# Kernel tuning notes

Measured on AMD Instinct MI355X. Metric: run time of the kernel, lower is better.

## Reference

```python
import jax, jax.numpy as jnp
import numpy as np

B, P, C = 2, 2048, 64
SIZE = 128          # image_size
K = 8               # points_per_pixel (z-buffer depth)
RADIUS = 1.5        # in pixels
RAD_POW = 2
TAU = 1.0
BIG = 1e10          # sentinel z for pixels a point does not cover


def setup_inputs() -> dict:
    key = jax.random.key(0)
    k1, k2, k3 = jax.random.split(key, 3)
    xy = jax.random.uniform(k1, (B, P, 2), minval=-1.0, maxval=1.0)   # NDC xy
    z = jax.random.uniform(k2, (B, P, 1), minval=0.1, maxval=10.0)    # depth > 0
    pts3D = jnp.concatenate([xy, z], axis=-1)                          # [B,P,3]
    src = jax.random.normal(k3, (B, C, P), dtype=jnp.float32)          # [B,C,P]
    return {"pts3D": pts3D, "src": src}


def reference(pts3D, src):
    # --- sign flips from the torch forward: pts[:, :, :2] *= -1 ---
    pts = pts3D * jnp.array([-1.0, -1.0, 1.0], dtype=pts3D.dtype)
    px, py, pz = pts[..., 0], pts[..., 1], pts[..., 2]                 # [B,P]

    r_ndc = float(RADIUS) / float(SIZE) * 2.0

    # pixel-center NDC grid (pytorch3d convention: +x left, +y up)
    ii = jnp.arange(SIZE, dtype=pts.dtype)
    ndc = 1.0 - 2.0 * (ii + 0.5) / SIZE                                # [SIZE]

    # squared NDC distance pixel->point: [B,H,W,P]
    dx = ndc[None, None, :, None] - px[:, None, None, :]               # [B,1,W,P]
    dy = ndc[None, :, None, None] - py[:, None, None, :]               # [B,H,1,P]
    d2 = dx * dx + dy * dy                                             # [B,H,W,P]

    # rasterize_points: per pixel, K nearest-in-z points within radius
    inside = d2 <= r_ndc * r_ndc
    zkey = jnp.where(inside, pz[:, None, None, :], jnp.asarray(BIG, d2.dtype))
    neg_top, idx = jax.lax.top_k(-zkey, K)            # smallest z first, [B,H,W,K]
    valid = (-neg_top) < BIG                           # idx >= 0 equivalent

    dist = jnp.take_along_axis(d2, idx, axis=-1)       # [B,H,W,K]
    dist = dist / (r_ndc ** RAD_POW)

    # alphas = (1 - clamp(dist,0.001,1)^0.5)^tau
    alphas = (1.0 - jnp.sqrt(jnp.clip(dist, 0.001, 1.0))) ** TAU
    alphas = jnp.where(valid, alphas, 0.0)

    # alpha_composite: w_k = a_k * prod_{j<k} (1 - a_j), front-to-back
    T = jnp.cumprod(1.0 - alphas, axis=-1)
    w = alphas * jnp.concatenate([jnp.ones_like(T[..., :1]), T[..., :-1]], axis=-1)

    # gather features per batch: src [B,C,P], idx [B,H,W,K] -> [B,C,H,W,K]
    gathered = jax.vmap(lambda f, i: f[:, i])(src, idx)
    out = jnp.einsum('bchwk,bhwk->bchw', gathered, w)  # [B,C,H,W]
    return out
```

## Files before the change

### kernel.cpp

```cpp
#include <hip/hip_runtime.h>
#include <hip/hip_bf16.h>

#define BATCH 2
#define NPTS 2048
#define NCH 64
#define IMG 128
#define KTOP 8
#define BIGF 1e10f
#define CAP 256

__global__ __launch_bounds__(256) void transpose_src(
    const float* __restrict__ src, float* __restrict__ srcT) {
  __shared__ float tile[64][65];
  int b = blockIdx.x >> 5;
  int p0 = (blockIdx.x & 31) << 6;
  int tx = threadIdx.x & 63;
  int ty = threadIdx.x >> 6;
  const float* s = src + b * NCH * NPTS;
  #pragma unroll
  for (int cc = 0; cc < 64; cc += 4) {
    int c = cc + ty;
    tile[tx][c] = s[c * NPTS + p0 + tx];
  }
  __syncthreads();
  float* dT = srcT + (b * NPTS + p0) * NCH;
  #pragma unroll
  for (int pp = 0; pp < 64; pp += 4) {
    int p = pp + ty;
    dT[p * NCH + tx] = tile[p][tx];
  }
}

__global__ __launch_bounds__(256) void raster_fused(
    const float* __restrict__ pts,
    const float* __restrict__ srcT,
    float* __restrict__ out) {
  __shared__ float4 cand[CAP];
  __shared__ int cnt_s;

  const int bid = blockIdx.x;
  const int b = bid >> 8;
  const int h = (bid >> 1) & 127;
  const int w0 = (bid & 1) << 6;
  const int tid = threadIdx.x;

  if (tid == 0) cnt_s = 0;
  __syncthreads();

  const float r_ndc = 0.0234375f;
  const float r2 = r_ndc * r_ndc;
  const float yc = 1.0f - 2.0f * (h + 0.5f) / 128.0f;

  const float* pb = pts + b * NPTS * 3;
  for (int p = tid; p < NPTS; p += 256) {
    float y = pb[p * 3 + 1];
    float dy = yc + y;
    if (dy * dy <= r2) {
      int pos = atomicAdd(&cnt_s, 1);
      if (pos < CAP)
        cand[pos] = make_float4(pb[p * 3 + 0], y, pb[p * 3 + 2],
                                __int_as_float(p));
    }
  }
  __syncthreads();
  const int cnt = min(cnt_s, CAP);

  const int pix = tid & 63;
  const int w = w0 + pix;
  const float xc = 1.0f - 2.0f * (w + 0.5f) / 128.0f;

  float bz[KTOP], bd[KTOP];
  int bi[KTOP];
  #pragma unroll
  for (int k = 0; k < KTOP; ++k) { bz[k] = BIGF; bd[k] = 0.f; bi[k] = 0x7fffffff; }

  for (int j = 0; j < cnt; ++j) {
    float4 c4 = cand[j];
    float dx = xc + c4.x;
    float dyy = yc + c4.y;
    float d2 = dx * dx + dyy * dyy;
    if (d2 <= r2) {
      float cz = c4.z, cd = d2;
      int ci = __float_as_int(c4.w);
      #pragma unroll
      for (int s = 0; s < KTOP; ++s) {
        bool lt = (cz < bz[s]) || (cz == bz[s] && ci < bi[s]);
        float tz = bz[s], td = bd[s];
        int ti = bi[s];
        if (lt) { bz[s] = cz; bd[s] = cd; bi[s] = ci; cz = tz; cd = td; ci = ti; }
      }
    }
  }

  float wgt[KTOP];
  float T = 1.0f;
  const float inv_r2 = 1.0f / r2;
  #pragma unroll
  for (int k = 0; k < KTOP; ++k) {
    float alpha = 0.0f;
    if (bz[k] < BIGF) {
      float dist = bd[k] * inv_r2;
      dist = fminf(fmaxf(dist, 0.001f), 1.0f);
      alpha = 1.0f - sqrtf(dist);
    } else {
      bi[k] = 0;
    }
    wgt[k] = alpha * T;
    T *= (1.0f - alpha);
  }

  const float4* sb = (const float4*)(srcT + b * NPTS * NCH);
  const float4* rows[KTOP];
  #pragma unroll
  for (int k = 0; k < KTOP; ++k) rows[k] = sb + bi[k] * (NCH / 4);

  const int cq0 = (tid >> 6) * 4;
  float* ob = out + (b * NCH * IMG + h) * IMG + w;
  #pragma unroll
  for (int q = 0; q < 4; ++q) {
    int cq = cq0 + q;
    float4 acc = {0.f, 0.f, 0.f, 0.f};
    #pragma unroll
    for (int k = 0; k < KTOP; ++k) {
      float4 v = rows[k][cq];
      acc.x += wgt[k] * v.x;
      acc.y += wgt[k] * v.y;
      acc.z += wgt[k] * v.z;
      acc.w += wgt[k] * v.w;
    }
    int c = cq * 4;
    ob[(c + 0) * (IMG * IMG)] = acc.x;
    ob[(c + 1) * (IMG * IMG)] = acc.y;
    ob[(c + 2) * (IMG * IMG)] = acc.z;
    ob[(c + 3) * (IMG * IMG)] = acc.w;
  }
}

extern "C" void kernel_launch(void* const* d_in, const int* in_sizes, int n_in,
                              void* d_out, int out_size, void* d_ws, size_t ws_size,
                              hipStream_t stream) {
  const float* pts = (const float*)d_in[0];
  const float* src = (const float*)d_in[1];
  float* out = (float*)d_out;
  float* srcT = (float*)d_ws;

  transpose_src<<<BATCH * (NPTS / 64), 256, 0, stream>>>(src, srcT);
  raster_fused<<<BATCH * IMG * 2, 256, 0, stream>>>(pts, srcT, out);
}
```

Baseline: 88.58 us.

## Drop transpose kernel; stage candidate features in shared memory per row block

Removes the separate transpose kernel and its launch. Each raster block now gathers the features of its candidate points directly from the channel-major src into a padded shared-memory table. The top-K tracking carries a local candidate index, so the final weighted sum reads from LDS instead of making scattered global loads. CAP drops to 128, which risks silently dropping candidates if a row band holds more points, and the strided global gather adds work to every block.

```diff
diff --git a/kernel.cpp b/kernel.cpp
--- a/kernel.cpp
+++ b/kernel.cpp
@@ -7,35 +7,15 @@
 #define IMG 128
 #define KTOP 8
 #define BIGF 1e10f
-#define CAP 256
-
-__global__ __launch_bounds__(256) void transpose_src(
-    const float* __restrict__ src, float* __restrict__ srcT) {
-  __shared__ float tile[64][65];
-  int b = blockIdx.x >> 5;
-  int p0 = (blockIdx.x & 31) << 6;
-  int tx = threadIdx.x & 63;
-  int ty = threadIdx.x >> 6;
-  const float* s = src + b * NCH * NPTS;
-  #pragma unroll
-  for (int cc = 0; cc < 64; cc += 4) {
-    int c = cc + ty;
-    tile[tx][c] = s[c * NPTS + p0 + tx];
-  }
-  __syncthreads();
-  float* dT = srcT + (b * NPTS + p0) * NCH;
-  #pragma unroll
-  for (int pp = 0; pp < 64; pp += 4) {
-    int p = pp + ty;
-    dT[p * NCH + tx] = tile[p][tx];
-  }
-}
+#define CAP 128
+#define FPITCH 68
 
 __global__ __launch_bounds__(256) void raster_fused(
     const float* __restrict__ pts,
-    const float* __restrict__ srcT,
+    const float* __restrict__ src,
     float* __restrict__ out) {
   __shared__ float4 cand[CAP];
+  __shared__ float feat[CAP * FPITCH];
   __shared__ int cnt_s;
 
   const int bid = blockIdx.x;
@@ -65,14 +45,26 @@
   __syncthreads();
   const int cnt = min(cnt_s, CAP);
 
+  const float* sbase = src + b * NCH * NPTS;
+  for (int t = tid; t < cnt * NCH; t += 256) {
+    int j = t >> 6;
+    int c = t & 63;
+    int p = __float_as_int(cand[j].w);
+    feat[j * FPITCH + c] = sbase[c * NPTS + p];
+  }
+  if (cnt == 0 && tid < NCH) feat[tid] = 0.0f;
+  __syncthreads();
+
   const int pix = tid & 63;
   const int w = w0 + pix;
   const float xc = 1.0f - 2.0f * (w + 0.5f) / 128.0f;
 
   float bz[KTOP], bd[KTOP];
-  int bi[KTOP];
+  int bi[KTOP], bj[KTOP];
   #pragma unroll
-  for (int k = 0; k < KTOP; ++k) { bz[k] = BIGF; bd[k] = 0.f; bi[k] = 0x7fffffff; }
+  for (int k = 0; k < KTOP; ++k) {
+    bz[k] = BIGF; bd[k] = 0.f; bi[k] = 0x7fffffff; bj[k] = 0;
+  }
 
   for (int j = 0; j < cnt; ++j) {
     float4 c4 = cand[j];
@@ -82,12 +74,16 @@
     if (d2 <= r2) {
       float cz = c4.z, cd = d2;
       int ci = __float_as_int(c4.w);
+      int cj = j;
       #pragma unroll
       for (int s = 0; s < KTOP; ++s) {
         bool lt = (cz < bz[s]) || (cz == bz[s] && ci < bi[s]);
         float tz = bz[s], td = bd[s];
-        int ti = bi[s];
-        if (lt) { bz[s] = cz; bd[s] = cd; bi[s] = ci; cz = tz; cd = td; ci = ti; }
+        int ti = bi[s], tj = bj[s];
+        if (lt) {
+          bz[s] = cz; bd[s] = cd; bi[s] = ci; bj[s] = cj;
+          cz = tz; cd = td; ci = ti; cj = tj;
+        }
       }
     }
   }
@@ -102,33 +98,30 @@
       float dist = bd[k] * inv_r2;
       dist = fminf(fmaxf(dist, 0.001f), 1.0f);
       alpha = 1.0f - sqrtf(dist);
-    } else {
-      bi[k] = 0;
     }
     wgt[k] = alpha * T;
     T *= (1.0f - alpha);
   }
 
-  const float4* sb = (const float4*)(srcT + b * NPTS * NCH);
-  const float4* rows[KTOP];
+  const int cq0 = (tid >> 6) * 4;
+  const float4* frows[KTOP];
   #pragma unroll
-  for (int k = 0; k < KTOP; ++k) rows[k] = sb + bi[k] * (NCH / 4);
+  for (int k = 0; k < KTOP; ++k)
+    frows[k] = (const float4*)&feat[bj[k] * FPITCH + cq0 * 4];
 
-  const int cq0 = (tid >> 6) * 4;
   float* ob = out + (b * NCH * IMG + h) * IMG + w;
   #pragma unroll
   for (int q = 0; q < 4; ++q) {
-    int cq = cq0 + q;
     float4 acc = {0.f, 0.f, 0.f, 0.f};
     #pragma unroll
     for (int k = 0; k < KTOP; ++k) {
-      float4 v = rows[k][cq];
+      float4 v = frows[k][q];
       acc.x += wgt[k] * v.x;
       acc.y += wgt[k] * v.y;
       acc.z += wgt[k] * v.z;
       acc.w += wgt[k] * v.w;
     }
-    int c = cq * 4;
+    int c = (cq0 + q) * 4;
     ob[(c + 0) * (IMG * IMG)] = acc.x;
     ob[(c + 1) * (IMG * IMG)] = acc.y;
     ob[(c + 2) * (IMG * IMG)] = acc.z;
@@ -142,8 +135,6 @@
   const float* pts = (const float*)d_in[0];
   const float* src = (const float*)d_in[1];
   float* out = (float*)d_out;
-  float* srcT = (float*)d_ws;
 
-  transpose_src<<<BATCH * (NPTS / 64), 256, 0, stream>>>(src, srcT);
-  raster_fused<<<BATCH * IMG * 2, 256, 0, stream>>>(pts, srcT, out);
+  raster_fused<<<BATCH * IMG * 2, 256, 0, stream>>>(pts, src, out);
 }
```

New measurement: 92.70 us. +4.6%, slower.

## Precompute per-row point bins in prep kernel and split raster by channel group

Applied to the files above, without the earlier changes.

Moves the per-row candidate filtering into a prep kernel that also does the src transpose. The prep kernel compacts candidates with a wave ballot and prefix count instead of shared atomics and writes them to global bins with per-row counts. The raster kernel now uses 64-thread blocks, one per 16-channel group, so there are 4x more blocks. Each block reloads that row's bins and repeats the K-nearest selection redundantly for its channel group. It also drops the index tie-break in the z sort and halves the bin capacity to 128, so candidates beyond that are dropped and equal-z ordering can differ.

```diff
diff --git a/kernel.cpp b/kernel.cpp
--- a/kernel.cpp
+++ b/kernel.cpp
@@ -7,72 +7,95 @@
 #define IMG 128
 #define KTOP 8
 #define BIGF 1e10f
-#define CAP 256
+#define CAP 128
 
-__global__ __launch_bounds__(256) void transpose_src(
-    const float* __restrict__ src, float* __restrict__ srcT) {
-  __shared__ float tile[64][65];
-  int b = blockIdx.x >> 5;
-  int p0 = (blockIdx.x & 31) << 6;
-  int tx = threadIdx.x & 63;
-  int ty = threadIdx.x >> 6;
-  const float* s = src + b * NCH * NPTS;
-  #pragma unroll
-  for (int cc = 0; cc < 64; cc += 4) {
-    int c = cc + ty;
-    tile[tx][c] = s[c * NPTS + p0 + tx];
-  }
-  __syncthreads();
-  float* dT = srcT + (b * NPTS + p0) * NCH;
-  #pragma unroll
-  for (int pp = 0; pp < 64; pp += 4) {
-    int p = pp + ty;
-    dT[p * NCH + tx] = tile[p][tx];
+__global__ __launch_bounds__(256) void prep(
+    const float* __restrict__ pts,
+    const float* __restrict__ src,
+    float* __restrict__ srcT,
+    float4* __restrict__ bins,
+    int* __restrict__ counts) {
+  const int blk = blockIdx.x;
+  if (blk < 64) {
+    __shared__ float tile[64][65];
+    int b = blk >> 5;
+    int p0 = (blk & 31) << 6;
+    int tx = threadIdx.x & 63;
+    int ty = threadIdx.x >> 6;
+    const float* s = src + b * NCH * NPTS;
+    #pragma unroll
+    for (int cc = 0; cc < 64; cc += 4) {
+      int c = cc + ty;
+      tile[tx][c] = s[c * NPTS + p0 + tx];
+    }
+    __syncthreads();
+    float* dT = srcT + (b * NPTS + p0) * NCH;
+    #pragma unroll
+    for (int pp = 0; pp < 64; pp += 4) {
+      int p = pp + ty;
+      dT[p * NCH + tx] = tile[p][tx];
+    }
+  } else {
+    const int wave = threadIdx.x >> 6;
+    const int lane = threadIdx.x & 63;
+    const int row = ((blk - 64) << 2) + wave;
+    const int b = row >> 7;
+    const int h = row & 127;
+    const float r_ndc = 0.0234375f;
+    const float r2 = r_ndc * r_ndc;
+    const float yc = 1.0f - 2.0f * (h + 0.5f) / 128.0f;
+    const float* pb = pts + b * NPTS * 3;
+    float4* brow = bins + row * CAP;
+    int base = 0;
+    for (int it = 0; it < NPTS / 64; ++it) {
+      int p = (it << 6) + lane;
+      float y = pb[p * 3 + 1];
+      float dy = yc + y;
+      bool hit = (dy * dy <= r2);
+      unsigned long long mask = __ballot(hit);
+      int prefix = __popcll(mask & ((1ull << lane) - 1ull));
+      if (hit) {
+        int pos = base + prefix;
+        if (pos < CAP)
+          brow[pos] = make_float4(pb[p * 3 + 0], y, pb[p * 3 + 2],
+                                  __int_as_float(p));
+      }
+      base += __popcll(mask);
+    }
+    if (lane == 0) counts[row] = min(base, CAP);
   }
 }
 
-__global__ __launch_bounds__(256) void raster_fused(
-    const float* __restrict__ pts,
+__global__ __launch_bounds__(64) void raster(
+    const float4* __restrict__ bins,
+    const int* __restrict__ counts,
     const float* __restrict__ srcT,
     float* __restrict__ out) {
   __shared__ float4 cand[CAP];
-  __shared__ int cnt_s;
 
   const int bid = blockIdx.x;
-  const int b = bid >> 8;
-  const int h = (bid >> 1) & 127;
-  const int w0 = (bid & 1) << 6;
-  const int tid = threadIdx.x;
+  const int cg = bid & 3;
+  const int half = (bid >> 2) & 1;
+  const int h = (bid >> 3) & 127;
+  const int b = bid >> 10;
+  const int lane = threadIdx.x;
 
-  if (tid == 0) cnt_s = 0;
+  const int row = (b << 7) + h;
+  const int cnt = min(counts[row], CAP);
+  const float4* grow = bins + row * CAP;
+  for (int j = lane; j < cnt; j += 64) cand[j] = grow[j];
   __syncthreads();
 
   const float r_ndc = 0.0234375f;
   const float r2 = r_ndc * r_ndc;
   const float yc = 1.0f - 2.0f * (h + 0.5f) / 128.0f;
-
-  const float* pb = pts + b * NPTS * 3;
-  for (int p = tid; p < NPTS; p += 256) {
-    float y = pb[p * 3 + 1];
-    float dy = yc + y;
-    if (dy * dy <= r2) {
-      int pos = atomicAdd(&cnt_s, 1);
-      if (pos < CAP)
-        cand[pos] = make_float4(pb[p * 3 + 0], y, pb[p * 3 + 2],
-                                __int_as_float(p));
-    }
-  }
-  __syncthreads();
-  const int cnt = min(cnt_s, CAP);
-
-  const int pix = tid & 63;
-  const int w = w0 + pix;
+  const int w = (half << 6) + lane;
   const float xc = 1.0f - 2.0f * (w + 0.5f) / 128.0f;
 
   float bz[KTOP], bd[KTOP];
-  int bi[KTOP];
+  int bp[KTOP];
   #pragma unroll
-  for (int k = 0; k < KTOP; ++k) { bz[k] = BIGF; bd[k] = 0.f; bi[k] = 0x7fffffff; }
+  for (int k = 0; k < KTOP; ++k) { bz[k] = BIGF; bd[k] = 0.f; bp[k] = 0; }
 
   for (int j = 0; j < cnt; ++j) {
     float4 c4 = cand[j];
@@ -81,13 +104,14 @@
     float d2 = dx * dx + dyy * dyy;
     if (d2 <= r2) {
       float cz = c4.z, cd = d2;
-      int ci = __float_as_int(c4.w);
+      int cp = __float_as_int(c4.w);
       #pragma unroll
       for (int s = 0; s < KTOP; ++s) {
-        bool lt = (cz < bz[s]) || (cz == bz[s] && ci < bi[s]);
+        bool lt = (cz < bz[s]);
         float tz = bz[s], td = bd[s];
-        int ti = bi[s];
-        if (lt) { bz[s] = cz; bd[s] = cd; bi[s] = ci; cz = tz; cd = td; ci = ti; }
+        int tp = bp[s];
+        if (lt) { bz[s] = cz; bd[s] = cd; bp[s] = cp;
+                  cz = tz; cd = td; cp = tp; }
       }
     }
   }
@@ -102,38 +126,30 @@
       float dist = bd[k] * inv_r2;
       dist = fminf(fmaxf(dist, 0.001f), 1.0f);
       alpha = 1.0f - sqrtf(dist);
-    } else {
-      bi[k] = 0;
     }
     wgt[k] = alpha * T;
     T *= (1.0f - alpha);
   }
 
-  const float4* sb = (const float4*)(srcT + b * NPTS * NCH);
-  const float4* rows[KTOP];
+  const float* sb = srcT + (size_t)b * NPTS * NCH + cg * 16;
+  float4 acc0 = {0,0,0,0}, acc1 = {0,0,0,0}, acc2 = {0,0,0,0}, acc3 = {0,0,0,0};
   #pragma unroll
-  for (int k = 0; k < KTOP; ++k) rows[k] = sb + bi[k] * (NCH / 4);
+  for (int k = 0; k < KTOP; ++k) {
+    const float4* fr = (const float4*)(sb + (size_t)bp[k] * NCH);
+    float wk = wgt[k];
+    float4 v0 = fr[0], v1 = fr[1], v2 = fr[2], v3 = fr[3];
+    acc0.x += wk * v0.x; acc0.y += wk * v0.y; acc0.z += wk * v0.z; acc0.w += wk * v0.w;
+    acc1.x += wk * v1.x; acc1.y += wk * v1.y; acc1.z += wk * v1.z; acc1.w += wk * v1.w;
+    acc2.x += wk * v2.x; acc2.y += wk * v2.y; acc2.z += wk * v2.z; acc2.w += wk * v2.w;
+    acc3.x += wk * v3.x; acc3.y += wk * v3.y; acc3.z += wk * v3.z; acc3.w += wk * v3.w;
+  }
 
-  const int cq0 = (tid >> 6) * 4;
-  float* ob = out + (b * NCH * IMG + h) * IMG + w;
-  #pragma unroll
-  for (int q = 0; q < 4; ++q) {
-    int cq = cq0 + q;
-    float4 acc = {0.f, 0.f, 0.f, 0.f};
-    #pragma unroll
-    for (int k = 0; k < KTOP; ++k) {
-      float4 v = rows[k][cq];
-      acc.x += wgt[k] * v.x;
-      acc.y += wgt[k] * v.y;
-      acc.z += wgt[k] * v.z;
-      acc.w += wgt[k] * v.w;
-    }
-    int c = cq * 4;
-    ob[(c + 0) * (IMG * IMG)] = acc.x;
-    ob[(c + 1) * (IMG * IMG)] = acc.y;
-    ob[(c + 2) * (IMG * IMG)] = acc.z;
-    ob[(c + 3) * (IMG * IMG)] = acc.w;
-  }
+  float* ob = out + (((size_t)b * NCH + cg * 16) * IMG + h) * IMG + w;
+  const int S = IMG * IMG;
+  ob[0 * S] = acc0.x;  ob[1 * S] = acc0.y;  ob[2 * S] = acc0.z;  ob[3 * S] = acc0.w;
+  ob[4 * S] = acc1.x;  ob[5 * S] = acc1.y;  ob[6 * S] = acc1.z;  ob[7 * S] = acc1.w;
+  ob[8 * S] = acc2.x;  ob[9 * S] = acc2.y;  ob[10 * S] = acc2.z; ob[11 * S] = acc2.w;
+  ob[12 * S] = acc3.x; ob[13 * S] = acc3.y; ob[14 * S] = acc3.z; ob[15 * S] = acc3.w;
 }
 
 extern "C" void kernel_launch(void* const* d_in, const int* in_sizes, int n_in,
@@ -142,8 +158,13 @@
   const float* pts = (const float*)d_in[0];
   const float* src = (const float*)d_in[1];
   float* out = (float*)d_out;
-  float* srcT = (float*)d_ws;
 
-  transpose_src<<<BATCH * (NPTS / 64), 256, 0, stream>>>(src, srcT);
-  raster_fused<<<BATCH * IMG * 2, 256, 0, stream>>>(pts, srcT, out);
+  char* ws = (char*)d_ws;
+  float* srcT = (float*)ws;
+  float4* bins = (float4*)(ws + (size_t)BATCH * NPTS * NCH * 4);
+  int* counts = (int*)(ws + (size_t)BATCH * NPTS * NCH * 4 +
+                       (size_t)BATCH * IMG * CAP * 16);
+
+  prep<<<128, 256, 0, stream>>>(pts, src, srcT, bins, counts);
+  raster<<<BATCH * IMG * 2 * 4, 64, 0, stream>>>(bins, counts, srcT, out);
 }
```

Result: faster. 86.02 us (-2.9%).
